# Kernel tuning notes

Hardware: AMD Instinct MI355X
Metric: run time of the kernel (lower is better)

## Reference

```python
import jax, jax.numpy as jnp
import numpy as np
from jax import lax

B, T, C, U = 32, 512, 4233, 64


def setup_inputs() -> dict:
    key = jax.random.key(0)
    k1, k2 = jax.random.split(key)
    logits = jax.random.normal(k1, (B, T, C), dtype=jnp.float32)
    ctc_logit = jax.nn.log_softmax(logits, axis=-1)  # [B, T, C] log-probs
    # labels in [1, C) so none equal blank (code treats blank-valued labels as pad)
    label = jax.random.randint(k2, (U, B), 1, C, dtype=jnp.int32)  # [U, B]
    return {"ctc_logit": ctc_logit, "label": label, "blank_id": 0}


def ctc_fa(ctc_logit, label, blank_id):
    pad_value = jnp.finfo(ctc_logit.dtype).min
    lab = label.T  # [B, U]
    lab = jnp.where(lab == blank_id, -1, lab)
    Bb, Uu = lab.shape
    Tt = ctc_logit.shape[1]
    Cc = ctc_logit.shape[2]
    yl = (lab >= 0).sum(1) * 2 + 1  # [B] extended label length
    # interleave blanks: [blank, l0, blank, l1, ..., blank] -> lab_T = 2U+1
    blanks = jnp.full_like(lab, blank_id)
    ext = jnp.stack([blanks, lab], axis=2).reshape(Bb, 2 * Uu)
    ext = jnp.pad(ext, ((0, 0), (0, 1)), constant_values=blank_id)  # [B, labT]
    labT = 2 * Uu + 1
    shifted2 = jnp.pad(ext, ((0, 0), (2, 0)), constant_values=-1)[:, :labT]
    cond = (ext == blank_id) | (ext == shifted2)  # [B, labT]
    ext_idx = ext % Cc  # mimic torch negative-index wrap for -1 pad labels
    # emission log-probs gathered per extended-label position: [B, T, labT]
    emit = jnp.take_along_axis(ctc_logit, ext_idx[:, None, :], axis=2)
    dp0 = jnp.full((Bb, labT), pad_value, ctc_logit.dtype)
    dp0 = dp0.at[:, 0].set(emit[:, 0, 0]).at[:, 1].set(emit[:, 0, 1])
    jrange = jnp.arange(labT)

    def shift(x, n):
        return jnp.pad(x, ((0, 0), (n, 0)), constant_values=pad_value)[:, :labT]

    def step(dp_prev, emit_t):
        s1 = shift(dp_prev, 1)
        s2 = shift(dp_prev, 2)
        a2 = jnp.stack([dp_prev, s1], axis=-1)          # [B, labT, 2]
        a3 = jnp.stack([dp_prev, s1, s2], axis=-1)      # [B, labT, 3]
        idx1 = jnp.argmax(a2, axis=-1)
        idx2 = jnp.argmax(a3, axis=-1)
        lse2 = jax.scipy.special.logsumexp(a2, axis=-1)
        lse3 = jax.scipy.special.logsumexp(a3, axis=-1)
        dp_t = emit_t + jnp.where(cond, lse2, lse3)
        bp_t = jrange[None, :] - jnp.where(cond, idx1, idx2)
        return dp_t, (dp_t, bp_t)

    emit_tbj = jnp.swapaxes(emit, 0, 1)  # [T, B, labT]
    dp_last, (_, bps) = lax.scan(step, dp0, emit_tbj[1:])
    bp0 = jnp.broadcast_to(jrange[None, None, :], (1, Bb, labT)).astype(bps.dtype)
    bp_all = jnp.concatenate([bp0, bps], axis=0)  # [T, B, labT]
    bi = jnp.arange(Bb)
    d1 = dp_last[bi, yl - 1]
    d2 = dp_last[bi, yl - 2]
    ctc_loss = -jnp.logaddexp(d1, d2)
    ctc_loss = 2 * ctc_loss / (yl - 1)
    # Viterbi backtrack -> hard alignment [B, T, labT]
    wi0 = jnp.where(d1 > d2, yl - 1, yl - 2)

    def bstep(wi, bp_t):
        align_t = (jrange[None, :] == wi[:, None]).astype(jnp.int32)
        wi_next = jnp.take_along_axis(bp_t, wi[:, None], axis=1)[:, 0]
        return wi_next, align_t

    _, align_ts = lax.scan(bstep, wi0, bp_all, reverse=True)  # [T, B, labT]
    align = jnp.swapaxes(align_ts, 0, 1)  # [B, T, labT]
    return align, ctc_loss


def reference(ctc_logit, label, blank_id):
    return ctc_fa(ctc_logit, label, blank_id)
```

## Files before the change

kernel.cpp:

```cpp
#include <hip/hip_runtime.h>
#include <math.h>

#define NB 32
#define NT 512
#define NC 4233
#define NU 64
#define LABT 129
#define PADV (-3.4028234663852886e38f)
#define SCANBLK 192

__global__ void ctc_prep_kernel(const int* __restrict__ label,
                                const int* __restrict__ blank_ptr,
                                int* __restrict__ ext_idx,
                                int* __restrict__ cond,
                                int* __restrict__ yl)
{
    const int b = blockIdx.x;
    const int j = threadIdx.x;
    const int blank = blank_ptr[0];

    if (j < 64) {
        int raw = label[j * NB + b];
        unsigned long long m = __ballot(raw != blank);
        if (j == 0) yl[b] = 2 * (int)__popcll(m) + 1;
    }

    if (j < LABT) {
        int extv;
        if ((j & 1) == 0) {
            extv = blank;
        } else {
            int raw = label[((j - 1) >> 1) * NB + b];
            extv = (raw == blank) ? -1 : raw;
        }
        int sh2;
        if (j < 2) {
            sh2 = -1;
        } else if (((j - 2) & 1) == 0) {
            sh2 = blank;
        } else {
            int raw2 = label[((j - 3) >> 1) * NB + b];
            sh2 = (raw2 == blank) ? -1 : raw2;
        }
        int c = (extv == blank) || (extv == sh2);
        int idx = extv % NC;
        if (idx < 0) idx += NC;
        ext_idx[b * LABT + j] = idx;
        cond[b * LABT + j]    = c;
    }
}

__global__ __launch_bounds__(SCANBLK)
void ctc_scan_kernel(const float* __restrict__ logit,
                     const int*   __restrict__ ext_idx,
                     const int*   __restrict__ cond,
                     const int*   __restrict__ yl,
                     int*   __restrict__ wout,
                     float* __restrict__ loss_out)
{
    __shared__ float dbuf[2][SCANBLK + 8];
    __shared__ unsigned long long bpm[NT][3][2];
    __shared__ int wl[NT];

    const int b = blockIdx.x;
    const int j = threadIdx.x;
    const bool act = (j < LABT);

    const int col = act ? ext_idx[b * LABT + j] : 0;
    const int cnd = act ? cond[b * LABT + j] : 1;

    const float* lb = logit + (size_t)b * NT * NC;

    float* pa = dbuf[0];
    float* pb = dbuf[1];

    float e0 = lb[col];
    pa[j] = (j <= 1) ? e0 : PADV;

    float r0 = lb[(size_t)1 * NC + col];
    float r1 = lb[(size_t)2 * NC + col];
    float r2 = lb[(size_t)3 * NC + col];
    float r3 = lb[(size_t)4 * NC + col];
    __syncthreads();

#define STEP(tcur, rr, tload)                                                  \
    do {                                                                       \
        float a  = pa[j];                                                      \
        float b1 = (j >= 1) ? pa[j - 1] : PADV;                                \
        float c2 = (j >= 2) ? pa[j - 2] : PADV;                                \
        float c2e = cnd ? PADV : c2;      \
        float m  = fmaxf(fmaxf(a, b1), c2e);                                   \
        float lse = m + logf(expf(a - m) + expf(b1 - m) + expf(c2e - m));      \
        int delta = (a >= b1 && a >= c2e) ? 0 : ((b1 >= c2e) ? 1 : 2);         \
        pb[j] = rr + lse;                                                      \
        unsigned long long mm0 = __ballot(delta & 1);                          \
        unsigned long long mm1 = __ballot(delta >> 1);                         \
        if ((j & 63) == 0) {                                                   \
            bpm[tcur][j >> 6][0] = mm0;                                        \
            bpm[tcur][j >> 6][1] = mm1;                                        \
        }                                                                      \
        if ((tload) < NT) rr = lb[(size_t)(tload) * NC + col];                 \
        __syncthreads();                                                       \
        float* tpp = pa; pa = pb; pb = tpp;                                    \
    } while (0)

    int t = 1;
    for (; t + 3 < NT; t += 4) {
        STEP(t,     r0, t + 4);
        STEP(t + 1, r1, t + 5);
        STEP(t + 2, r2, t + 6);
        STEP(t + 3, r3, t + 7);
    }
    STEP(t,     r0, NT);
    STEP(t + 1, r1, NT);
    STEP(t + 2, r2, NT);
#undef STEP

    if (j == 0) {
        int Y = yl[b];
        float d1 = pa[Y - 1];
        float d2 = pa[Y - 2];
        float mm = fmaxf(d1, d2);
        float la = mm + logf(expf(d1 - mm) + expf(d2 - mm));
        loss_out[b] = -la * 2.0f / (float)(Y - 1);

        int w = (d1 > d2) ? (Y - 1) : (Y - 2);
        for (int tt = NT - 1; tt >= 1; --tt) {
            wl[tt] = w;
            int wv = w >> 6, ln = w & 63;
            unsigned long long m0 = bpm[tt][wv][0];
            unsigned long long m1 = bpm[tt][wv][1];
            int dd = (int)((m0 >> ln) & 1ULL) + 2 * (int)((m1 >> ln) & 1ULL);
            w -= dd;
        }
        wl[0] = w;
    }
    __syncthreads();
    for (int tt = j; tt < NT; tt += SCANBLK) wout[b * NT + tt] = wl[tt];
}

__global__ void ctc_align_kernel(const int* __restrict__ w,
                                 float* __restrict__ out)
{
    int tid = blockIdx.x * blockDim.x + threadIdx.x;
    if (tid >= NB * NT * LABT) return;
    int j  = tid % LABT;
    int bt = tid / LABT;
    out[tid] = (j == w[bt]) ? 1.0f : 0.0f;
}

extern "C" void kernel_launch(void* const* d_in, const int* in_sizes, int n_in,
                              void* d_out, int out_size, void* d_ws, size_t ws_size,
                              hipStream_t stream)
{
    const float* logit = (const float*)d_in[0];
    const int*   label = (const int*)d_in[1];
    const int*   blank = (const int*)d_in[2];

    float* out = (float*)d_out;
    int*   ws  = (int*)d_ws;

    int* ext_idx = ws;
    int* cond    = ws + NB * LABT;
    int* yl      = ws + 2 * NB * LABT;
    int* w       = ws + 2 * NB * LABT + NB;

    ctc_prep_kernel<<<NB, SCANBLK, 0, stream>>>(label, blank, ext_idx, cond, yl);
    ctc_scan_kernel<<<NB, SCANBLK, 0, stream>>>(logit, ext_idx, cond, yl, w,
                                                out + NB * NT * LABT);
    int total = NB * NT * LABT;
    ctc_align_kernel<<<(total + 255) / 256, 256, 0, stream>>>(w, out);
}
```

Measured before the change: 490.0 us.

## Pre-gather emissions and run CTC scan in a single wavefront with shuffles

Adds a fully parallel gather kernel that collects the per-position emission log-probs into a compact interleaved buffer. The sequential scan then runs as one 64-lane wavefront per batch, with each lane owning two label positions plus a broadcast last position. Neighbour values move through shuffles instead of shared memory, which removes the per-timestep __syncthreads. Prefetch depth grows to 8 timesteps and label prep is folded into the scan. The cost is an extra gathered buffer round-trip through memory, and the buffer falls back to the output region when the workspace is small.

```diff
diff --git a/kernel.cpp b/kernel.cpp
--- a/kernel.cpp
+++ b/kernel.cpp
@@ -7,136 +7,177 @@
 #define NU 64
 #define LABT 129
 #define PADV (-3.4028234663852886e38f)
-#define SCANBLK 192
-
-__global__ void ctc_prep_kernel(const int* __restrict__ label,
-                                const int* __restrict__ blank_ptr,
-                                int* __restrict__ ext_idx,
-                                int* __restrict__ cond,
-                                int* __restrict__ yl)
-{
-    const int b = blockIdx.x;
-    const int j = threadIdx.x;
-    const int blank = blank_ptr[0];
-
-    if (j < 64) {
-        int raw = label[j * NB + b];
-        unsigned long long m = __ballot(raw != blank);
-        if (j == 0) yl[b] = 2 * (int)__popcll(m) + 1;
+
+
+__device__ __forceinline__ int extcol(int c, const int* label, int b, int blank) {
+    if ((c & 1) == 0) return blank;
+    int raw = label[((c - 1) >> 1) * NB + b];
+    int e = (raw == blank) ? -1 : raw;
+    int idx = e % NC;
+    if (idx < 0) idx += NC;
+    return idx;
+}
+
+__device__ __forceinline__ int condcell(int c, const int* label, int b, int blank) {
+    if ((c & 1) == 0) return 1;
+    int u = (c - 1) >> 1;
+    int raw = label[u * NB + b];
+    int e = (raw == blank) ? -1 : raw;
+    int s2;
+    if (u == 0) s2 = -1;
+    else {
+        int raw2 = label[(u - 1) * NB + b];
+        s2 = (raw2 == blank) ? -1 : raw2;
     }
-
-    if (j < LABT) {
-        int extv;
-        if ((j & 1) == 0) {
-            extv = blank;
-        } else {
-            int raw = label[((j - 1) >> 1) * NB + b];
-            extv = (raw == blank) ? -1 : raw;
-        }
-        int sh2;
-        if (j < 2) {
-            sh2 = -1;
-        } else if (((j - 2) & 1) == 0) {
-            sh2 = blank;
-        } else {
-            int raw2 = label[((j - 3) >> 1) * NB + b];
-            sh2 = (raw2 == blank) ? -1 : raw2;
-        }
-        int c = (extv == blank) || (extv == sh2);
-        int idx = extv % NC;
-        if (idx < 0) idx += NC;
-        ext_idx[b * LABT + j] = idx;
-        cond[b * LABT + j]    = c;
-    }
-}
-
-__global__ __launch_bounds__(SCANBLK)
-void ctc_scan_kernel(const float* __restrict__ logit,
-                     const int*   __restrict__ ext_idx,
-                     const int*   __restrict__ cond,
-                     const int*   __restrict__ yl,
+    return (e == blank) || (e == s2);
+}
+
+__global__ void ctc_gather_kernel(const float* __restrict__ logit,
+                                  const int*   __restrict__ label,
+                                  const int*   __restrict__ blank_ptr,
+                                  float* __restrict__ emit)
+{
+    int tid = blockIdx.x * blockDim.x + threadIdx.x;
+    int blank = blank_ptr[0];
+    int k = tid & 127;
+    int bt = tid >> 7;
+    int b  = bt >> 9;
+    int c  = (k & 1) ? 64 + (k >> 1) : (k >> 1);
+    int col = extcol(c, label, b, blank);
+    emit[tid] = logit[(size_t)bt * NC + col];
+}
+
+__global__ __launch_bounds__(64)
+void ctc_scan_kernel(const float* __restrict__ emitb,
+                     const int*   __restrict__ label,
+                     const int*   __restrict__ blank_ptr,
                      int*   __restrict__ wout,
                      float* __restrict__ loss_out)
 {
-    __shared__ float dbuf[2][SCANBLK + 8];
-    __shared__ unsigned long long bpm[NT][3][2];
-    __shared__ int wl[NT];
+    __shared__ unsigned long long bpm[NT][4];
+    __shared__ unsigned char     bp2s[NT];
+    __shared__ float             dpfin[132];
+    __shared__ int               wl[NT];
 
     const int b = blockIdx.x;
-    const int j = threadIdx.x;
-    const bool act = (j < LABT);
-
-    const int col = act ? ext_idx[b * LABT + j] : 0;
-    const int cnd = act ? cond[b * LABT + j] : 1;
-
-    const float* lb = logit + (size_t)b * NT * NC;
-
-    float* pa = dbuf[0];
-    float* pb = dbuf[1];
-
-    float e0 = lb[col];
-    pa[j] = (j <= 1) ? e0 : PADV;
-
-    float r0 = lb[(size_t)1 * NC + col];
-    float r1 = lb[(size_t)2 * NC + col];
-    float r2 = lb[(size_t)3 * NC + col];
-    float r3 = lb[(size_t)4 * NC + col];
+    const int l = threadIdx.x;
+    const int blank = blank_ptr[0];
+
+    int rawl = label[l * NB + b];
+    unsigned long long ylm = __ballot(rawl != blank);
+    const int Y = 2 * (int)__popcll(ylm) + 1;
+
+    const int cnd0 = condcell(l,      label, b, blank);
+    const int cnd1 = condcell(64 + l, label, b, blank);
+
+    const int lm1 = (l + 63) & 63;
+    const int lm2 = (l + 62) & 63;
+
+    const float2* emrow = (const float2*)emitb + (size_t)b * NT * 64 + l;
+
+    float2 e00 = emrow[0];
+    float dp0 = (l <= 1) ? e00.x : PADV;
+    float dp1 = PADV;
+    float dp2 = PADV;
+
+    float2 r0 = emrow[(size_t)1 * 64];
+    float2 r1 = emrow[(size_t)2 * 64];
+    float2 r2 = emrow[(size_t)3 * 64];
+    float2 r3 = emrow[(size_t)4 * 64];
+    float2 r4 = emrow[(size_t)5 * 64];
+    float2 r5 = emrow[(size_t)6 * 64];
+    float2 r6 = emrow[(size_t)7 * 64];
+    float2 r7 = emrow[(size_t)8 * 64];
+
+#define STEP(tcur, rr, tload)                                                   \
+    do {                                                                         \
+        float a0 = dp0, a1 = dp1, a2 = dp2;                                      \
+        float q1_0 = __shfl(a0, lm1);                       \
+        float q2_0 = __shfl(a0, lm2);                                            \
+        float q1_1 = __shfl(a1, lm1);                                            \
+        float q2_1 = __shfl(a1, lm2);                                            \
+        float s0m1 = (l >= 1) ? q1_0 : PADV;                                     \
+        float s0m2 = (l >= 2) ? q2_0 : PADV;                                     \
+        float s1m1 = (l == 0) ? q1_0 : q1_1;                 \
+        float s1m2 = (l <= 1) ? q2_0 : q2_1;  \
+        float c0 = cnd0 ? PADV : s0m2;                                           \
+        float c1 = cnd1 ? PADV : s1m2;                                           \
+        float m0 = fmaxf(fmaxf(a0, s0m1), c0);                                   \
+        float z0 = m0 + logf(expf(a0 - m0) + expf(s0m1 - m0) + expf(c0 - m0));   \
+        int   d0 = (a0 >= s0m1 && a0 >= c0) ? 0 : ((s0m1 >= c0) ? 1 : 2);        \
+        float m1v = fmaxf(fmaxf(a1, s1m1), c1);                                  \
+        float z1 = m1v + logf(expf(a1 - m1v) + expf(s1m1 - m1v) + expf(c1 - m1v));\
+        int   d1 = (a1 >= s1m1 && a1 >= c1) ? 0 : ((s1m1 >= c1) ? 1 : 2);        \
+        float m2 = fmaxf(a2, a1);                 \
+        float z2 = m2 + logf(expf(a2 - m2) + expf(a1 - m2));                     \
+        int   d2 = (a2 >= a1) ? 0 : 1;                                           \
+        float e2 = __int_as_float(__builtin_amdgcn_readfirstlane(                \
+                       __float_as_int(rr.x)));      \
+        dp0 = rr.x + z0;                                                         \
+        dp1 = rr.y + z1;                                                         \
+        dp2 = e2   + z2;                                                         \
+        unsigned long long b00 = __ballot(d0 & 1);                               \
+        unsigned long long b01 = __ballot(d0 >> 1);                              \
+        unsigned long long b10 = __ballot(d1 & 1);                               \
+        unsigned long long b11 = __ballot(d1 >> 1);                              \
+        if (l == 0) {                                                            \
+            bpm[tcur][0] = b00; bpm[tcur][1] = b01;                              \
+            bpm[tcur][2] = b10; bpm[tcur][3] = b11;                              \
+        }                                                                        \
+        if (l == 63) bp2s[tcur] = (unsigned char)d2;                             \
+        if ((tload) <= NT - 1) rr = emrow[(size_t)(tload) * 64];                 \
+    } while (0)
+
+    int t = 1;
+    for (; t + 7 <= NT - 1; t += 8) {
+        STEP(t,     r0, t + 8);
+        STEP(t + 1, r1, t + 9);
+        STEP(t + 2, r2, t + 10);
+        STEP(t + 3, r3, t + 11);
+        STEP(t + 4, r4, t + 12);
+        STEP(t + 5, r5, t + 13);
+        STEP(t + 6, r6, t + 14);
+        STEP(t + 7, r7, t + 15);
+    }
+    STEP(t,     r0, NT); t++;
+    STEP(t,     r1, NT); t++;
+    STEP(t,     r2, NT); t++;
+    STEP(t,     r3, NT); t++;
+    STEP(t,     r4, NT); t++;
+    STEP(t,     r5, NT); t++;
+    STEP(t,     r6, NT);
+#undef STEP
+
+    dpfin[l] = dp0;
+    dpfin[64 + l] = dp1;
+    if (l == 63) dpfin[128] = dp2;
     __syncthreads();
 
-#define STEP(tcur, rr, tload)                                                  \
-    do {                                                                       \
-        float a  = pa[j];                                                      \
-        float b1 = (j >= 1) ? pa[j - 1] : PADV;                                \
-        float c2 = (j >= 2) ? pa[j - 2] : PADV;                                \
-        float c2e = cnd ? PADV : c2;      \
-        float m  = fmaxf(fmaxf(a, b1), c2e);                                   \
-        float lse = m + logf(expf(a - m) + expf(b1 - m) + expf(c2e - m));      \
-        int delta = (a >= b1 && a >= c2e) ? 0 : ((b1 >= c2e) ? 1 : 2);         \
-        pb[j] = rr + lse;                                                      \
-        unsigned long long mm0 = __ballot(delta & 1);                          \
-        unsigned long long mm1 = __ballot(delta >> 1);                         \
-        if ((j & 63) == 0) {                                                   \
-            bpm[tcur][j >> 6][0] = mm0;                                        \
-            bpm[tcur][j >> 6][1] = mm1;                                        \
-        }                                                                      \
-        if ((tload) < NT) rr = lb[(size_t)(tload) * NC + col];                 \
-        __syncthreads();                                                       \
-        float* tpp = pa; pa = pb; pb = tpp;                                    \
-    } while (0)
-
-    int t = 1;
-    for (; t + 3 < NT; t += 4) {
-        STEP(t,     r0, t + 4);
-        STEP(t + 1, r1, t + 5);
-        STEP(t + 2, r2, t + 6);
-        STEP(t + 3, r3, t + 7);
-    }
-    STEP(t,     r0, NT);
-    STEP(t + 1, r1, NT);
-    STEP(t + 2, r2, NT);
-#undef STEP
-
-    if (j == 0) {
-        int Y = yl[b];
-        float d1 = pa[Y - 1];
-        float d2 = pa[Y - 2];
-        float mm = fmaxf(d1, d2);
-        float la = mm + logf(expf(d1 - mm) + expf(d2 - mm));
+    if (l == 0) {
+        float d1v = dpfin[Y - 1];
+        float d2v = dpfin[Y - 2];
+        float mm = fmaxf(d1v, d2v);
+        float la = mm + logf(expf(d1v - mm) + expf(d2v - mm));
         loss_out[b] = -la * 2.0f / (float)(Y - 1);
 
-        int w = (d1 > d2) ? (Y - 1) : (Y - 2);
+        int w = (d1v > d2v) ? (Y - 1) : (Y - 2);
+#pragma unroll 4
         for (int tt = NT - 1; tt >= 1; --tt) {
             wl[tt] = w;
-            int wv = w >> 6, ln = w & 63;
-            unsigned long long m0 = bpm[tt][wv][0];
-            unsigned long long m1 = bpm[tt][wv][1];
-            int dd = (int)((m0 >> ln) & 1ULL) + 2 * (int)((m1 >> ln) & 1ULL);
+            unsigned long long w0lo = bpm[tt][0], w1lo = bpm[tt][1];
+            unsigned long long w0hi = bpm[tt][2], w1hi = bpm[tt][3];
+            int dd2 = (int)bp2s[tt];
+            unsigned long long m0 = (w < 64) ? w0lo : w0hi;
+            unsigned long long m1 = (w < 64) ? w1lo : w1hi;
+            int sh = w & 63;
+            int dd = (int)((m0 >> sh) & 1ULL) + 2 * (int)((m1 >> sh) & 1ULL);
+            if (w == 128) dd = dd2;
             w -= dd;
         }
         wl[0] = w;
     }
     __syncthreads();
-    for (int tt = j; tt < NT; tt += SCANBLK) wout[b * NT + tt] = wl[tt];
+    for (int tt = l; tt < NT; tt += 64) wout[b * NT + tt] = wl[tt];
 }
 
 __global__ void ctc_align_kernel(const int* __restrict__ w,
@@ -160,14 +201,15 @@
     float* out = (float*)d_out;
     int*   ws  = (int*)d_ws;
 
-    int* ext_idx = ws;
-    int* cond    = ws + NB * LABT;
-    int* yl      = ws + 2 * NB * LABT;
-    int* w       = ws + 2 * NB * LABT + NB;
-
-    ctc_prep_kernel<<<NB, SCANBLK, 0, stream>>>(label, blank, ext_idx, cond, yl);
-    ctc_scan_kernel<<<NB, SCANBLK, 0, stream>>>(logit, ext_idx, cond, yl, w,
-                                                out + NB * NT * LABT);
+    int*   wout = ws;
+    size_t emit_elems = (size_t)NB * NT * 128;
+    bool   use_ws = ws_size >= (size_t)NB * NT * 4 + emit_elems * 4 + 256;
+    float* emit = use_ws ? (float*)(ws + NB * NT) : out;
+
+    ctc_gather_kernel<<<(int)(emit_elems / 256), 256, 0, stream>>>(
+        logit, label, blank, emit);
+    ctc_scan_kernel<<<NB, 64, 0, stream>>>(emit, label, blank, wout,
+                                           out + (size_t)NB * NT * LABT);
     int total = NB * NT * LABT;
-    ctc_align_kernel<<<(total + 255) / 256, 256, 0, stream>>>(w, out);
-}
+    ctc_align_kernel<<<(total + 255) / 256, 256, 0, stream>>>(wout, out);
+}
```

After: 633.0 us. +29.2%, slower.
